# Performance work log

Hardware: AMD Instinct MI355X
Metric: run time of the kernel (lower is better)

## Reference

```python
import jax, jax.numpy as jnp
import numpy as np

NUM_CLASSES = 4
SMOOTH = 1e-05
W_DICE, W_CE, W_BOUND = 1.0, 1.0, 0.01
BIG = 1e8  # effectively-infinite squared distance


def _edt_sq_pass(f, axis):
    # Exact 1D squared-distance transform along `axis` via min-plus:
    # out[i] = min_j f[j] + (i-j)^2  (brute-force O(n^2), fully vectorized)
    n = f.shape[axis]
    i = jnp.arange(n, dtype=f.dtype)
    d2 = (i[:, None] - i[None, :]) ** 2  # [n, n]
    fm = jnp.moveaxis(f, axis, -1)
    out = jnp.min(fm[..., None, :] + d2, axis=-1)
    return jnp.moveaxis(out, -1, axis)


def _edt(zero_mask):
    # Euclidean distance to the nearest True voxel of zero_mask
    # (equivalent to scipy distance_transform_edt(~zero_mask)'s convention:
    #  distance to nearest zero of the input == nearest True of zero_mask).
    f = jnp.where(zero_mask, 0.0, BIG).astype(jnp.float32)
    for ax in range(f.ndim):
        f = _edt_sq_pass(f, ax)
    return jnp.sqrt(f)


def _signed_distance(mask):
    # mask: bool [D,H,W]; signed distance map: + outside, - inside.
    d_out = _edt(mask)            # distance(1 - mask)
    d_in = _edt(~mask)            # distance(mask)
    sdf = d_out - d_in
    total = jnp.sum(mask)
    size = mask.size
    sdf = jnp.where(total == 0, jnp.ones_like(sdf), sdf)
    sdf = jnp.where(total == size, -jnp.ones_like(sdf), sdf)
    return sdf


def setup_inputs() -> dict:
    key = jax.random.key(0)
    k1, k2 = jax.random.split(key)
    preds = jax.random.normal(k1, (4, NUM_CLASSES, 64, 64, 64), dtype=jnp.float32)
    targets = jax.random.randint(k2, (4, 64, 64, 64), 0, NUM_CLASSES, dtype=jnp.int32)
    return {"preds": preds, "targets": targets}


def reference(preds, targets):
    B = preds.shape[0]
    probs = jax.nn.softmax(preds, axis=1)  # [B,C,D,H,W]

    # --- Soft Dice ---
    onehot = jax.nn.one_hot(targets, NUM_CLASSES, dtype=preds.dtype)  # [B,D,H,W,C]
    onehot = jnp.moveaxis(onehot, -1, 1)  # [B,C,D,H,W]
    inter = jnp.sum(probs * onehot, axis=(2, 3, 4))
    union = jnp.sum(probs, axis=(2, 3, 4)) + jnp.sum(onehot, axis=(2, 3, 4))
    dice = (2.0 * inter + SMOOTH) / (union + SMOOTH)
    l_dice = 1.0 - jnp.mean(dice)

    # --- Cross entropy (mean over all voxels) ---
    logp = jax.nn.log_softmax(preds, axis=1)
    picked = jnp.take_along_axis(logp, targets[:, None].astype(jnp.int32), axis=1)
    l_ce = -jnp.mean(picked)

    # --- Boundary loss (classes 1..C-1) ---
    l_bound = jnp.float32(0.0)
    for c in range(1, NUM_CLASSES):
        mask_c = targets == c  # [B,D,H,W]
        sdf_c = jax.vmap(_signed_distance)(mask_c)  # [B,D,H,W]
        l_bound = l_bound + jnp.sum(jnp.mean(sdf_c * probs[:, c], axis=(1, 2, 3)))
    l_bound = l_bound / (B * (NUM_CLASSES - 1))

    return W_DICE * l_dice + W_CE * l_ce + W_BOUND * l_bound
```

## Files before the change

### kernel.cpp

```cpp
#include <hip/hip_runtime.h>
#include <hip/hip_bf16.h>
#include <math.h>

#define NVOX 262144
#define BIGF 1e8f
#define GRID_A 1024
#define GRID_B 768
#define GRID_K2 768

__device__ __forceinline__ unsigned short f2bf(float x) {
    __hip_bfloat16 h = __float2bfloat16(x);
    return *reinterpret_cast<unsigned short*>(&h);
}
__device__ __forceinline__ float bf2f(unsigned short u) {
    __hip_bfloat16 h = *reinterpret_cast<__hip_bfloat16*>(&u);
    return __bfloat162float(h);
}
__device__ __forceinline__ unsigned short dist2_u16(unsigned long long mask, int w) {
    if (mask == 0ull) return 0xFFFFu;
    unsigned long long mr = mask >> w;
    unsigned long long ml = mask << (63 - w);
    int dr = mr ? __builtin_ctzll(mr) : 127;
    int dl = ml ? __builtin_clzll(ml) : 127;
    int dd = dr < dl ? dr : dl;
    return (unsigned short)(dd * dd);
}

__global__ __launch_bounds__(256) void K1_fused(
    const float* __restrict__ preds, const int* __restrict__ targets,
    unsigned short* __restrict__ bufA, unsigned short* __restrict__ probsT,
    float* __restrict__ part_stats) {
    __shared__ float tO[64 * 65];
    __shared__ float tI[64 * 65];
    __shared__ float sred[4 * 13];
    int bid = blockIdx.x;
    int t = threadIdx.x, lane = t & 63, wid = t >> 6;

    if (bid < GRID_A) {
        int b = bid >> 8, seg = bid & 255;
        size_t vbase = (size_t)seg * 1024 + 4 * t;
        const float* p = preds + (size_t)(b * 4) * NVOX + vbase;
        float4 x0 = *(const float4*)(p);
        float4 x1 = *(const float4*)(p + NVOX);
        float4 x2 = *(const float4*)(p + 2 * NVOX);
        float4 x3 = *(const float4*)(p + 3 * NVOX);
        int4 tv4 = *(const int4*)(targets + (size_t)b * NVOX + vbase);

        float q[13];
        #pragma unroll
        for (int k = 0; k < 13; ++k) q[k] = 0.0f;
        unsigned short pb[3][4];

        #pragma unroll
        for (int j = 0; j < 4; ++j) {
            float a0 = (&x0.x)[j], a1 = (&x1.x)[j], a2 = (&x2.x)[j], a3 = (&x3.x)[j];
            int tv = (&tv4.x)[j];
            float m  = fmaxf(fmaxf(a0, a1), fmaxf(a2, a3));
            float e0 = expf(a0 - m), e1 = expf(a1 - m), e2 = expf(a2 - m), e3 = expf(a3 - m);
            float ssum = e0 + e1 + e2 + e3;
            float inv  = 1.0f / ssum;
            float p0 = e0 * inv, p1 = e1 * inv, p2 = e2 * inv, p3 = e3 * inv;
            float xt = (tv == 0) ? a0 : (tv == 1) ? a1 : (tv == 2) ? a2 : a3;
            q[12] += -(xt - m - logf(ssum));
            q[4] += p0; q[5] += p1; q[6] += p2; q[7] += p3;
            if (tv == 0)      { q[0] += p0; q[8]  += 1.0f; }
            else if (tv == 1) { q[1] += p1; q[9]  += 1.0f; }
            else if (tv == 2) { q[2] += p2; q[10] += 1.0f; }
            else              { q[3] += p3; q[11] += 1.0f; }
            pb[0][j] = f2bf(p1); pb[1][j] = f2bf(p2); pb[2][j] = f2bf(p3);
        }

        int v0 = (int)vbase;
        int d = v0 >> 12, h = (v0 >> 6) & 63, w0 = v0 & 63;
        size_t poff = (size_t)h * 4096 + d * 64 + w0;
        #pragma unroll
        for (int c = 0; c < 3; ++c) {
            ushort4 u = make_ushort4(pb[c][0], pb[c][1], pb[c][2], pb[c][3]);
            *(ushort4*)(probsT + (size_t)(b * 3 + c) * NVOX + poff) = u;
        }

        #pragma unroll
        for (int k = 0; k < 13; ++k) {
            float x = q[k];
            #pragma unroll
            for (int o = 32; o > 0; o >>= 1) x += __shfl_down(x, o);
            if (lane == 0) sred[wid * 13 + k] = x;
        }
        __syncthreads();
        if (t < 13) {
            float s = sred[t] + sred[13 + t] + sred[26 + t] + sred[39 + t];
            part_stats[t * 1024 + bid] = s;
        }
    } else {
        int blk = bid - GRID_A;
        int cm = blk % 3;
        int bd = blk / 3;
        int d = bd & 63, b = bd >> 6;
        int c = cm + 1;
        const int* tg = targets + (size_t)b * NVOX + (size_t)d * 4096;

        #pragma unroll
        for (int i = 0; i < 16; ++i) {
            int e = t + 256 * i;
            int h = wid + 4 * i;
            int tv = tg[e];
            unsigned long long mask = __ballot(tv == c);
            unsigned short o  = dist2_u16(mask, lane);
            unsigned short ii = dist2_u16(~mask, lane);
            tO[h * 65 + lane] = (o  == 0xFFFFu) ? BIGF : (float)o;
            tI[h * 65 + lane] = (ii == 0xFFFFu) ? BIGF : (float)ii;
        }
        __syncthreads();

        for (int r = 0; r < 16; ++r) {
            int w = wid * 16 + r;
            {
                float best = tO[lane * 65 + w];
                for (int dk = 1; dk < 64; ++dk) {
                    float d2 = (float)(dk * dk);
                    if (__all(d2 >= best)) break;
                    int hl = lane - dk; hl = hl < 0 ? 0 : hl;
                    int hr = lane + dk; hr = hr > 63 ? 63 : hr;
                    best = fminf(fminf(best, tO[hl * 65 + w] + d2), tO[hr * 65 + w] + d2);
                }
                tO[lane * 65 + w] = best;
            }
            {
                float best = tI[lane * 65 + w];
                for (int dk = 1; dk < 64; ++dk) {
                    float d2 = (float)(dk * dk);
                    if (__all(d2 >= best)) break;
                    int hl = lane - dk; hl = hl < 0 ? 0 : hl;
                    int hr = lane + dk; hr = hr > 63 ? 63 : hr;
                    best = fminf(fminf(best, tI[hl * 65 + w] + d2), tI[hr * 65 + w] + d2);
                }
                tI[lane * 65 + w] = best;
            }
        }
        __syncthreads();

        int combo = b * 3 + cm;
        size_t oO = (size_t)combo * NVOX + (size_t)d * 64;
        size_t oI = (size_t)(combo + 12) * NVOX + (size_t)d * 64;
        #pragma unroll
        for (int i = 0; i < 16; ++i) {
            int h = wid + 4 * i;
            float vo = tO[h * 65 + lane];
            float vi = tI[h * 65 + lane];
            bufA[oO + (size_t)h * 4096 + lane] = (vo >= 1e7f) ? 0xFFFFu : (unsigned short)vo;
            bufA[oI + (size_t)h * 4096 + lane] = (vi >= 1e7f) ? 0xFFFFu : (unsigned short)vi;
        }
    }
}

__global__ __launch_bounds__(512) void K2_edt3_sdf(
    const unsigned short* __restrict__ bufA, const unsigned short* __restrict__ probsT,
    float* __restrict__ part_bound) {
    __shared__ float pl[2][64 * 65];
    __shared__ float sredb[8];
    int blk = blockIdx.x;
    int combo = blk >> 6, h = blk & 63;
    int t = threadIdx.x, lane = t & 63, wid = t >> 6;

    for (int v = 0; v < 2; ++v) {
        const unsigned short* src = bufA + (size_t)(combo + 12 * v) * NVOX + (size_t)h * 4096;
        #pragma unroll
        for (int i = 0; i < 8; ++i) {
            int e = t + 512 * i;
            unsigned short u = src[e];
            pl[v][e + (e >> 6)] = (u == 0xFFFFu) ? BIGF : (float)u;
        }
    }
    __syncthreads();

    for (int v = 0; v < 2; ++v) {
        for (int r = 0; r < 8; ++r) {
            int w = wid * 8 + r;
            float* col = &pl[v][w];
            float best = col[lane * 65];
            for (int dk = 1; dk < 64; ++dk) {
                float d2 = (float)(dk * dk);
                if (__all(d2 >= best)) break;
                int dl = lane - dk; dl = dl < 0 ? 0 : dl;
                int dr = lane + dk; dr = dr > 63 ? 63 : dr;
                best = fminf(fminf(best, col[dl * 65] + d2), col[dr * 65] + d2);
            }
            col[lane * 65] = best;
        }
    }
    __syncthreads();

    const unsigned short* pp = probsT + (size_t)combo * NVOX + (size_t)h * 4096;
    float acc = 0.0f;
    #pragma unroll
    for (int i = 0; i < 8; ++i) {
        int e = t + 512 * i;
        int li = e + (e >> 6);
        float sdf = sqrtf(pl[0][li]) - sqrtf(pl[1][li]);
        acc += sdf * bf2f(pp[e]);
    }
    #pragma unroll
    for (int o = 32; o > 0; o >>= 1) acc += __shfl_down(acc, o);
    if (lane == 0) sredb[wid] = acc;
    __syncthreads();
    if (t == 0) {
        float s = 0.0f;
        for (int j = 0; j < 8; ++j) s += sredb[j];
        part_bound[blk] = s;
    }
}

__global__ __launch_bounds__(1024) void K3_final(
    const float* __restrict__ part_stats, const float* __restrict__ part_bound,
    float* __restrict__ out) {
    __shared__ float sred[13 * 16];
    __shared__ float bred[12];
    __shared__ double S[52];
    int t = threadIdx.x, lane = t & 63, wid = t >> 6;

    float v[13];
    #pragma unroll
    for (int k = 0; k < 13; ++k) v[k] = part_stats[k * 1024 + t];
    float bv = (wid < 12) ? part_bound[wid * 64 + lane] : 0.0f;

    #pragma unroll
    for (int k = 0; k < 13; ++k) {
        float x = v[k];
        #pragma unroll
        for (int o = 32; o > 0; o >>= 1) x += __shfl_down(x, o);
        if (lane == 0) sred[k * 16 + wid] = x;
    }
    #pragma unroll
    for (int o = 32; o > 0; o >>= 1) bv += __shfl_down(bv, o);
    if (lane == 0 && wid < 12) bred[wid] = bv;
    __syncthreads();

    if (t < 52) {
        int k = t >> 2, b = t & 3;
        S[k * 4 + b] = (double)sred[k * 16 + b * 4]     + (double)sred[k * 16 + b * 4 + 1]
                     + (double)sred[k * 16 + b * 4 + 2] + (double)sred[k * 16 + b * 4 + 3];
    }
    __syncthreads();
    if (t == 0) {
        const double NV = (double)NVOX;
        double dice_sum = 0.0;
        for (int b = 0; b < 4; ++b)
            for (int c = 0; c < 4; ++c) {
                double inter = S[c * 4 + b];
                double un    = S[(4 + c) * 4 + b] + S[(8 + c) * 4 + b];
                dice_sum += (2.0 * inter + 1e-5) / (un + 1e-5);
            }
        double l_dice = 1.0 - dice_sum / 16.0;
        double l_ce = (S[48] + S[49] + S[50] + S[51]) / (4.0 * NV);
        double lb = 0.0;
        for (int cb = 0; cb < 12; ++cb) {
            int b = cb / 3, c = cb % 3 + 1;
            double cnt = S[(8 + c) * 4 + b];
            double s;
            if (cnt == 0.0)      s =  S[(4 + c) * 4 + b];
            else if (cnt == NV)  s = -S[(4 + c) * 4 + b];
            else                 s =  (double)bred[cb];
            lb += s / NV;
        }
        lb /= 12.0;
        out[0] = (float)(l_dice + l_ce + 0.01 * lb);
    }
}

extern "C" void kernel_launch(void* const* d_in, const int* in_sizes, int n_in,
                              void* d_out, int out_size, void* d_ws, size_t ws_size,
                              hipStream_t stream) {
    const float* preds   = (const float*)d_in[0];
    const int*   targets = (const int*)d_in[1];
    float* out = (float*)d_out;

    unsigned short* bufA   = (unsigned short*)d_ws;
    unsigned short* probsT = bufA + (size_t)24 * NVOX;
    float* part_stats = (float*)(probsT + (size_t)12 * NVOX);
    float* part_bound = part_stats + 13 * 1024;

    K1_fused<<<GRID_A + GRID_B, 256, 0, stream>>>(preds, targets, bufA, probsT, part_stats);
    K2_edt3_sdf<<<GRID_K2, 512, 0, stream>>>(bufA, probsT, part_bound);
    K3_final<<<1, 1024, 0, stream>>>(part_stats, part_bound, out);
}
```

Baseline: 48.82 us.

## Split fused stats/EDT kernel into two launches with finer stats grid

Splits the combined softmax-stats and first-two-axis EDT kernel into two separate kernels. The stats kernel now processes 2 voxels per thread across 2048 blocks, and uses exp2f, log2f and the hardware reciprocal in place of expf, logf and division. The final reduction kernel is adapted to 2048 partial sums per statistic. The aim is more parallelism and cheaper transcendentals in the stats pass. In exchange the two workloads can no longer overlap inside one launch, and the extra kernel launch is serialized.

```diff
diff --git a/kernel.cpp b/kernel.cpp
--- a/kernel.cpp
+++ b/kernel.cpp
@@ -4,7 +4,7 @@
 
 #define NVOX 262144
 #define BIGF 1e8f
-#define GRID_A 1024
+#define GRID_A 2048
 #define GRID_B 768
 #define GRID_K2 768
 
@@ -26,130 +26,135 @@
     return (unsigned short)(dd * dd);
 }
 
-__global__ __launch_bounds__(256) void K1_fused(
+__global__ __launch_bounds__(256) void kA2_stats_probs(
     const float* __restrict__ preds, const int* __restrict__ targets,
-    unsigned short* __restrict__ bufA, unsigned short* __restrict__ probsT,
-    float* __restrict__ part_stats) {
+    unsigned short* __restrict__ probsT, float* __restrict__ part_stats) {
+    __shared__ float sred[4 * 13];
+    int bid = blockIdx.x;
+    int t = threadIdx.x, lane = t & 63, wid = t >> 6;
+    int g0 = bid * 512 + 2 * t;
+    int b = g0 >> 18;
+    int v0 = g0 & (NVOX - 1);
+    const float* p = preds + (size_t)(b * 4) * NVOX + v0;
+    float2 x0 = *(const float2*)(p);
+    float2 x1 = *(const float2*)(p + NVOX);
+    float2 x2 = *(const float2*)(p + 2 * NVOX);
+    float2 x3 = *(const float2*)(p + 3 * NVOX);
+    int2 tv2 = *(const int2*)(targets + (size_t)b * NVOX + v0);
+
+    const float L2E = 1.4426950408889634f;
+    const float LN2 = 0.6931471805599453f;
+    float q[13];
+    #pragma unroll
+    for (int k = 0; k < 13; ++k) q[k] = 0.0f;
+    unsigned short pb[3][2];
+
+    #pragma unroll
+    for (int j = 0; j < 2; ++j) {
+        float a0 = (&x0.x)[j], a1 = (&x1.x)[j], a2 = (&x2.x)[j], a3 = (&x3.x)[j];
+        int tv = (&tv2.x)[j];
+        float m  = fmaxf(fmaxf(a0, a1), fmaxf(a2, a3));
+        float e0 = exp2f((a0 - m) * L2E);
+        float e1 = exp2f((a1 - m) * L2E);
+        float e2 = exp2f((a2 - m) * L2E);
+        float e3 = exp2f((a3 - m) * L2E);
+        float ssum = e0 + e1 + e2 + e3;
+        float inv  = __builtin_amdgcn_rcpf(ssum);
+        float p0 = e0 * inv, p1 = e1 * inv, p2 = e2 * inv, p3 = e3 * inv;
+        float xt = (tv == 0) ? a0 : (tv == 1) ? a1 : (tv == 2) ? a2 : a3;
+        q[12] += (m - xt) + log2f(ssum) * LN2;
+        q[4] += p0; q[5] += p1; q[6] += p2; q[7] += p3;
+        if (tv == 0)      { q[0] += p0; q[8]  += 1.0f; }
+        else if (tv == 1) { q[1] += p1; q[9]  += 1.0f; }
+        else if (tv == 2) { q[2] += p2; q[10] += 1.0f; }
+        else              { q[3] += p3; q[11] += 1.0f; }
+        pb[0][j] = f2bf(p1); pb[1][j] = f2bf(p2); pb[2][j] = f2bf(p3);
+    }
+
+    int d = v0 >> 12, h = (v0 >> 6) & 63, w0 = v0 & 63;
+    size_t poff = (size_t)h * 4096 + d * 64 + w0;
+    #pragma unroll
+    for (int c = 0; c < 3; ++c) {
+        ushort2 u = make_ushort2(pb[c][0], pb[c][1]);
+        *(ushort2*)(probsT + (size_t)(b * 3 + c) * NVOX + poff) = u;
+    }
+
+    #pragma unroll
+    for (int k = 0; k < 13; ++k) {
+        float x = q[k];
+        #pragma unroll
+        for (int o = 32; o > 0; o >>= 1) x += __shfl_down(x, o);
+        if (lane == 0) sred[wid * 13 + k] = x;
+    }
+    __syncthreads();
+    if (t < 13) {
+        float s = sred[t] + sred[13 + t] + sred[26 + t] + sred[39 + t];
+        part_stats[t * 2048 + bid] = s;
+    }
+}
+
+__global__ __launch_bounds__(256) void kB_edt12(
+    const int* __restrict__ targets, unsigned short* __restrict__ bufA) {
     __shared__ float tO[64 * 65];
     __shared__ float tI[64 * 65];
-    __shared__ float sred[4 * 13];
-    int bid = blockIdx.x;
-    int t = threadIdx.x, lane = t & 63, wid = t >> 6;
-
-    if (bid < GRID_A) {
-        int b = bid >> 8, seg = bid & 255;
-        size_t vbase = (size_t)seg * 1024 + 4 * t;
-        const float* p = preds + (size_t)(b * 4) * NVOX + vbase;
-        float4 x0 = *(const float4*)(p);
-        float4 x1 = *(const float4*)(p + NVOX);
-        float4 x2 = *(const float4*)(p + 2 * NVOX);
-        float4 x3 = *(const float4*)(p + 3 * NVOX);
-        int4 tv4 = *(const int4*)(targets + (size_t)b * NVOX + vbase);
-
-        float q[13];
-        #pragma unroll
-        for (int k = 0; k < 13; ++k) q[k] = 0.0f;
-        unsigned short pb[3][4];
-
-        #pragma unroll
-        for (int j = 0; j < 4; ++j) {
-            float a0 = (&x0.x)[j], a1 = (&x1.x)[j], a2 = (&x2.x)[j], a3 = (&x3.x)[j];
-            int tv = (&tv4.x)[j];
-            float m  = fmaxf(fmaxf(a0, a1), fmaxf(a2, a3));
-            float e0 = expf(a0 - m), e1 = expf(a1 - m), e2 = expf(a2 - m), e3 = expf(a3 - m);
-            float ssum = e0 + e1 + e2 + e3;
-            float inv  = 1.0f / ssum;
-            float p0 = e0 * inv, p1 = e1 * inv, p2 = e2 * inv, p3 = e3 * inv;
-            float xt = (tv == 0) ? a0 : (tv == 1) ? a1 : (tv == 2) ? a2 : a3;
-            q[12] += -(xt - m - logf(ssum));
-            q[4] += p0; q[5] += p1; q[6] += p2; q[7] += p3;
-            if (tv == 0)      { q[0] += p0; q[8]  += 1.0f; }
-            else if (tv == 1) { q[1] += p1; q[9]  += 1.0f; }
-            else if (tv == 2) { q[2] += p2; q[10] += 1.0f; }
-            else              { q[3] += p3; q[11] += 1.0f; }
-            pb[0][j] = f2bf(p1); pb[1][j] = f2bf(p2); pb[2][j] = f2bf(p3);
-        }
-
-        int v0 = (int)vbase;
-        int d = v0 >> 12, h = (v0 >> 6) & 63, w0 = v0 & 63;
-        size_t poff = (size_t)h * 4096 + d * 64 + w0;
-        #pragma unroll
-        for (int c = 0; c < 3; ++c) {
-            ushort4 u = make_ushort4(pb[c][0], pb[c][1], pb[c][2], pb[c][3]);
-            *(ushort4*)(probsT + (size_t)(b * 3 + c) * NVOX + poff) = u;
-        }
-
-        #pragma unroll
-        for (int k = 0; k < 13; ++k) {
-            float x = q[k];
-            #pragma unroll
-            for (int o = 32; o > 0; o >>= 1) x += __shfl_down(x, o);
-            if (lane == 0) sred[wid * 13 + k] = x;
-        }
-        __syncthreads();
-        if (t < 13) {
-            float s = sred[t] + sred[13 + t] + sred[26 + t] + sred[39 + t];
-            part_stats[t * 1024 + bid] = s;
-        }
-    } else {
-        int blk = bid - GRID_A;
-        int cm = blk % 3;
-        int bd = blk / 3;
-        int d = bd & 63, b = bd >> 6;
-        int c = cm + 1;
-        const int* tg = targets + (size_t)b * NVOX + (size_t)d * 4096;
-
-        #pragma unroll
-        for (int i = 0; i < 16; ++i) {
-            int e = t + 256 * i;
-            int h = wid + 4 * i;
-            int tv = tg[e];
-            unsigned long long mask = __ballot(tv == c);
-            unsigned short o  = dist2_u16(mask, lane);
-            unsigned short ii = dist2_u16(~mask, lane);
-            tO[h * 65 + lane] = (o  == 0xFFFFu) ? BIGF : (float)o;
-            tI[h * 65 + lane] = (ii == 0xFFFFu) ? BIGF : (float)ii;
-        }
-        __syncthreads();
-
-        for (int r = 0; r < 16; ++r) {
-            int w = wid * 16 + r;
-            {
-                float best = tO[lane * 65 + w];
-                for (int dk = 1; dk < 64; ++dk) {
-                    float d2 = (float)(dk * dk);
-                    if (__all(d2 >= best)) break;
-                    int hl = lane - dk; hl = hl < 0 ? 0 : hl;
-                    int hr = lane + dk; hr = hr > 63 ? 63 : hr;
-                    best = fminf(fminf(best, tO[hl * 65 + w] + d2), tO[hr * 65 + w] + d2);
-                }
-                tO[lane * 65 + w] = best;
-            }
-            {
-                float best = tI[lane * 65 + w];
-                for (int dk = 1; dk < 64; ++dk) {
-                    float d2 = (float)(dk * dk);
-                    if (__all(d2 >= best)) break;
-                    int hl = lane - dk; hl = hl < 0 ? 0 : hl;
-                    int hr = lane + dk; hr = hr > 63 ? 63 : hr;
-                    best = fminf(fminf(best, tI[hl * 65 + w] + d2), tI[hr * 65 + w] + d2);
-                }
-                tI[lane * 65 + w] = best;
-            }
-        }
-        __syncthreads();
-
-        int combo = b * 3 + cm;
-        size_t oO = (size_t)combo * NVOX + (size_t)d * 64;
-        size_t oI = (size_t)(combo + 12) * NVOX + (size_t)d * 64;
-        #pragma unroll
-        for (int i = 0; i < 16; ++i) {
-            int h = wid + 4 * i;
-            float vo = tO[h * 65 + lane];
-            float vi = tI[h * 65 + lane];
-            bufA[oO + (size_t)h * 4096 + lane] = (vo >= 1e7f) ? 0xFFFFu : (unsigned short)vo;
-            bufA[oI + (size_t)h * 4096 + lane] = (vi >= 1e7f) ? 0xFFFFu : (unsigned short)vi;
-        }
+    int blk = blockIdx.x;
+    int cm = blk % 3;
+    int bd = blk / 3;
+    int d = bd & 63, b = bd >> 6;
+    int c = cm + 1;
+    int t = threadIdx.x, lane = t & 63, wid = t >> 6;
+    const int* tg = targets + (size_t)b * NVOX + (size_t)d * 4096;
+
+    #pragma unroll
+    for (int i = 0; i < 16; ++i) {
+        int e = t + 256 * i;
+        int h = wid + 4 * i;
+        int tv = tg[e];
+        unsigned long long mask = __ballot(tv == c);
+        unsigned short o  = dist2_u16(mask, lane);
+        unsigned short ii = dist2_u16(~mask, lane);
+        tO[h * 65 + lane] = (o  == 0xFFFFu) ? BIGF : (float)o;
+        tI[h * 65 + lane] = (ii == 0xFFFFu) ? BIGF : (float)ii;
+    }
+    __syncthreads();
+
+    for (int r = 0; r < 16; ++r) {
+        int w = wid * 16 + r;
+        {
+            float best = tO[lane * 65 + w];
+            for (int dk = 1; dk < 64; ++dk) {
+                float d2 = (float)(dk * dk);
+                if (__all(d2 >= best)) break;
+                int hl = lane - dk; hl = hl < 0 ? 0 : hl;
+                int hr = lane + dk; hr = hr > 63 ? 63 : hr;
+                best = fminf(fminf(best, tO[hl * 65 + w] + d2), tO[hr * 65 + w] + d2);
+            }
+            tO[lane * 65 + w] = best;
+        }
+        {
+            float best = tI[lane * 65 + w];
+            for (int dk = 1; dk < 64; ++dk) {
+                float d2 = (float)(dk * dk);
+                if (__all(d2 >= best)) break;
+                int hl = lane - dk; hl = hl < 0 ? 0 : hl;
+                int hr = lane + dk; hr = hr > 63 ? 63 : hr;
+                best = fminf(fminf(best, tI[hl * 65 + w] + d2), tI[hr * 65 + w] + d2);
+            }
+            tI[lane * 65 + w] = best;
+        }
+    }
+    __syncthreads();
+
+    int combo = b * 3 + cm;
+    size_t oO = (size_t)combo * NVOX + (size_t)d * 64;
+    size_t oI = (size_t)(combo + 12) * NVOX + (size_t)d * 64;
+    #pragma unroll
+    for (int i = 0; i < 16; ++i) {
+        int h = wid + 4 * i;
+        float vo = tO[h * 65 + lane];
+        float vi = tI[h * 65 + lane];
+        bufA[oO + (size_t)h * 4096 + lane] = (vo >= 1e7f) ? 0xFFFFu : (unsigned short)vo;
+        bufA[oI + (size_t)h * 4096 + lane] = (vi >= 1e7f) ? 0xFFFFu : (unsigned short)vi;
     }
 }
 
@@ -213,22 +218,26 @@
 __global__ __launch_bounds__(1024) void K3_final(
     const float* __restrict__ part_stats, const float* __restrict__ part_bound,
     float* __restrict__ out) {
-    __shared__ float sred[13 * 16];
+    __shared__ float sredA[13 * 16];
+    __shared__ float sredB[13 * 16];
     __shared__ float bred[12];
     __shared__ double S[52];
     int t = threadIdx.x, lane = t & 63, wid = t >> 6;
 
-    float v[13];
-    #pragma unroll
-    for (int k = 0; k < 13; ++k) v[k] = part_stats[k * 1024 + t];
+    float vA[13], vB[13];
+    #pragma unroll
+    for (int k = 0; k < 13; ++k) {
+        vA[k] = part_stats[k * 2048 + t];
+        vB[k] = part_stats[k * 2048 + 1024 + t];
+    }
     float bv = (wid < 12) ? part_bound[wid * 64 + lane] : 0.0f;
 
     #pragma unroll
     for (int k = 0; k < 13; ++k) {
-        float x = v[k];
+        float xa = vA[k], xb = vB[k];
         #pragma unroll
-        for (int o = 32; o > 0; o >>= 1) x += __shfl_down(x, o);
-        if (lane == 0) sred[k * 16 + wid] = x;
+        for (int o = 32; o > 0; o >>= 1) { xa += __shfl_down(xa, o); xb += __shfl_down(xb, o); }
+        if (lane == 0) { sredA[k * 16 + wid] = xa; sredB[k * 16 + wid] = xb; }
     }
     #pragma unroll
     for (int o = 32; o > 0; o >>= 1) bv += __shfl_down(bv, o);
@@ -236,9 +245,12 @@
     __syncthreads();
 
     if (t < 52) {
-        int k = t >> 2, b = t & 3;
-        S[k * 4 + b] = (double)sred[k * 16 + b * 4]     + (double)sred[k * 16 + b * 4 + 1]
-                     + (double)sred[k * 16 + b * 4 + 2] + (double)sred[k * 16 + b * 4 + 3];
+        int k = t >> 2, bsel = t & 3;
+        const float* src = (bsel < 2) ? sredA : sredB;
+        int base = k * 16 + (bsel & 1) * 8;
+        double s = 0.0;
+        for (int j = 0; j < 8; ++j) s += (double)src[base + j];
+        S[k * 4 + bsel] = s;
     }
     __syncthreads();
     if (t == 0) {
@@ -277,9 +289,10 @@
     unsigned short* bufA   = (unsigned short*)d_ws;
     unsigned short* probsT = bufA + (size_t)24 * NVOX;
     float* part_stats = (float*)(probsT + (size_t)12 * NVOX);
-    float* part_bound = part_stats + 13 * 1024;
-
-    K1_fused<<<GRID_A + GRID_B, 256, 0, stream>>>(preds, targets, bufA, probsT, part_stats);
+    float* part_bound = part_stats + 13 * 2048;
+
+    kA2_stats_probs<<<GRID_A, 256, 0, stream>>>(preds, targets, probsT, part_stats);
+    kB_edt12<<<GRID_B, 256, 0, stream>>>(targets, bufA);
     K2_edt3_sdf<<<GRID_K2, 512, 0, stream>>>(bufA, probsT, part_bound);
     K3_final<<<1, 1024, 0, stream>>>(part_stats, part_bound, out);
 }
```

After: 58.47 us. +19.8%, slower.

## Split fused K1 into probs, stats and EDT kernels with u16 shared tiles

Applied to the files above, without the earlier changes.

Splits the heterogeneous fused first kernel into three kernels: one writing the bf16 transposed probabilities, one computing the dice/CE statistics, and one doing the first two EDT passes. The EDT tiles move from float to unsigned short in shared memory, which halves LDS use. The 0xFFFF sentinel is now kept as 65535 rather than mapped to a large float. Softmax uses exp2f and the hardware reciprocal. The split re-reads preds twice and adds launch overhead. It also changes how the sentinel distance behaves in later passes, which risks wrong results when a class is absent in a row.

```diff
diff --git a/kernel.cpp b/kernel.cpp
--- a/kernel.cpp
+++ b/kernel.cpp
@@ -4,7 +4,6 @@
 
 #define NVOX 262144
 #define BIGF 1e8f
-#define GRID_A 1024
 #define GRID_B 768
 #define GRID_K2 768
 
@@ -26,130 +25,158 @@
     return (unsigned short)(dd * dd);
 }
 
-__global__ __launch_bounds__(256) void K1_fused(
+__global__ __launch_bounds__(256) void kA_probs(
+    const float* __restrict__ preds, unsigned short* __restrict__ probsT) {
+    int bid = blockIdx.x, t = threadIdx.x;
+    int g0 = bid * 1024 + 4 * t;
+    int b = g0 >> 18;
+    int v0 = g0 & (NVOX - 1);
+    const float* p = preds + (size_t)(b * 4) * NVOX + v0;
+    float4 x0 = *(const float4*)(p);
+    float4 x1 = *(const float4*)(p + NVOX);
+    float4 x2 = *(const float4*)(p + 2 * NVOX);
+    float4 x3 = *(const float4*)(p + 3 * NVOX);
+
+    const float L2E = 1.4426950408889634f;
+    unsigned short pb[3][4];
+    #pragma unroll
+    for (int j = 0; j < 4; ++j) {
+        float a0 = (&x0.x)[j], a1 = (&x1.x)[j], a2 = (&x2.x)[j], a3 = (&x3.x)[j];
+        float m  = fmaxf(fmaxf(a0, a1), fmaxf(a2, a3));
+        float e0 = exp2f((a0 - m) * L2E);
+        float e1 = exp2f((a1 - m) * L2E);
+        float e2 = exp2f((a2 - m) * L2E);
+        float e3 = exp2f((a3 - m) * L2E);
+        float inv = __builtin_amdgcn_rcpf(e0 + e1 + e2 + e3);
+        pb[0][j] = f2bf(e1 * inv);
+        pb[1][j] = f2bf(e2 * inv);
+        pb[2][j] = f2bf(e3 * inv);
+    }
+    int d = v0 >> 12, h = (v0 >> 6) & 63, w0 = v0 & 63;
+    size_t poff = (size_t)h * 4096 + d * 64 + w0;
+    #pragma unroll
+    for (int c = 0; c < 3; ++c) {
+        ushort4 u = make_ushort4(pb[c][0], pb[c][1], pb[c][2], pb[c][3]);
+        *(ushort4*)(probsT + (size_t)(b * 3 + c) * NVOX + poff) = u;
+    }
+}
+
+__global__ __launch_bounds__(256) void kA_stats(
     const float* __restrict__ preds, const int* __restrict__ targets,
-    unsigned short* __restrict__ bufA, unsigned short* __restrict__ probsT,
     float* __restrict__ part_stats) {
-    __shared__ float tO[64 * 65];
-    __shared__ float tI[64 * 65];
     __shared__ float sred[4 * 13];
-    int bid = blockIdx.x;
+    int bid = blockIdx.x, t = threadIdx.x, lane = t & 63, wid = t >> 6;
+    int g0 = bid * 1024 + 4 * t;
+    int b = g0 >> 18;
+    int v0 = g0 & (NVOX - 1);
+    const float* p = preds + (size_t)(b * 4) * NVOX + v0;
+    float4 x0 = *(const float4*)(p);
+    float4 x1 = *(const float4*)(p + NVOX);
+    float4 x2 = *(const float4*)(p + 2 * NVOX);
+    float4 x3 = *(const float4*)(p + 3 * NVOX);
+    int4 tv4 = *(const int4*)(targets + (size_t)b * NVOX + v0);
+
+    const float L2E = 1.4426950408889634f;
+    const float LN2 = 0.6931471805599453f;
+    float q[13];
+    #pragma unroll
+    for (int k = 0; k < 13; ++k) q[k] = 0.0f;
+
+    #pragma unroll
+    for (int j = 0; j < 4; ++j) {
+        float a0 = (&x0.x)[j], a1 = (&x1.x)[j], a2 = (&x2.x)[j], a3 = (&x3.x)[j];
+        int tv = (&tv4.x)[j];
+        float m  = fmaxf(fmaxf(a0, a1), fmaxf(a2, a3));
+        float e0 = exp2f((a0 - m) * L2E);
+        float e1 = exp2f((a1 - m) * L2E);
+        float e2 = exp2f((a2 - m) * L2E);
+        float e3 = exp2f((a3 - m) * L2E);
+        float ssum = e0 + e1 + e2 + e3;
+        float inv  = __builtin_amdgcn_rcpf(ssum);
+        float p0 = e0 * inv, p1 = e1 * inv, p2 = e2 * inv, p3 = e3 * inv;
+        float xt = (tv == 0) ? a0 : (tv == 1) ? a1 : (tv == 2) ? a2 : a3;
+        q[12] += (m - xt) + log2f(ssum) * LN2;
+        q[4] += p0; q[5] += p1; q[6] += p2; q[7] += p3;
+        if (tv == 0)      { q[0] += p0; q[8]  += 1.0f; }
+        else if (tv == 1) { q[1] += p1; q[9]  += 1.0f; }
+        else if (tv == 2) { q[2] += p2; q[10] += 1.0f; }
+        else              { q[3] += p3; q[11] += 1.0f; }
+    }
+
+    #pragma unroll
+    for (int k = 0; k < 13; ++k) {
+        float x = q[k];
+        #pragma unroll
+        for (int o = 32; o > 0; o >>= 1) x += __shfl_down(x, o);
+        if (lane == 0) sred[wid * 13 + k] = x;
+    }
+    __syncthreads();
+    if (t < 13) {
+        float s = sred[t] + sred[13 + t] + sred[26 + t] + sred[39 + t];
+        part_stats[t * 1024 + bid] = s;
+    }
+}
+
+__global__ __launch_bounds__(256) void kB_edt12(
+    const int* __restrict__ targets, unsigned short* __restrict__ bufA) {
+    __shared__ unsigned short tO[64 * 66];
+    __shared__ unsigned short tI[64 * 66];
+    int blk = blockIdx.x;
+    int cm = blk % 3;
+    int bd = blk / 3;
+    int d = bd & 63, b = bd >> 6;
+    int c = cm + 1;
     int t = threadIdx.x, lane = t & 63, wid = t >> 6;
-
-    if (bid < GRID_A) {
-        int b = bid >> 8, seg = bid & 255;
-        size_t vbase = (size_t)seg * 1024 + 4 * t;
-        const float* p = preds + (size_t)(b * 4) * NVOX + vbase;
-        float4 x0 = *(const float4*)(p);
-        float4 x1 = *(const float4*)(p + NVOX);
-        float4 x2 = *(const float4*)(p + 2 * NVOX);
-        float4 x3 = *(const float4*)(p + 3 * NVOX);
-        int4 tv4 = *(const int4*)(targets + (size_t)b * NVOX + vbase);
-
-        float q[13];
-        #pragma unroll
-        for (int k = 0; k < 13; ++k) q[k] = 0.0f;
-        unsigned short pb[3][4];
-
-        #pragma unroll
-        for (int j = 0; j < 4; ++j) {
-            float a0 = (&x0.x)[j], a1 = (&x1.x)[j], a2 = (&x2.x)[j], a3 = (&x3.x)[j];
-            int tv = (&tv4.x)[j];
-            float m  = fmaxf(fmaxf(a0, a1), fmaxf(a2, a3));
-            float e0 = expf(a0 - m), e1 = expf(a1 - m), e2 = expf(a2 - m), e3 = expf(a3 - m);
-            float ssum = e0 + e1 + e2 + e3;
-            float inv  = 1.0f / ssum;
-            float p0 = e0 * inv, p1 = e1 * inv, p2 = e2 * inv, p3 = e3 * inv;
-            float xt = (tv == 0) ? a0 : (tv == 1) ? a1 : (tv == 2) ? a2 : a3;
-            q[12] += -(xt - m - logf(ssum));
-            q[4] += p0; q[5] += p1; q[6] += p2; q[7] += p3;
-            if (tv == 0)      { q[0] += p0; q[8]  += 1.0f; }
-            else if (tv == 1) { q[1] += p1; q[9]  += 1.0f; }
-            else if (tv == 2) { q[2] += p2; q[10] += 1.0f; }
-            else              { q[3] += p3; q[11] += 1.0f; }
-            pb[0][j] = f2bf(p1); pb[1][j] = f2bf(p2); pb[2][j] = f2bf(p3);
-        }
-
-        int v0 = (int)vbase;
-        int d = v0 >> 12, h = (v0 >> 6) & 63, w0 = v0 & 63;
-        size_t poff = (size_t)h * 4096 + d * 64 + w0;
-        #pragma unroll
-        for (int c = 0; c < 3; ++c) {
-            ushort4 u = make_ushort4(pb[c][0], pb[c][1], pb[c][2], pb[c][3]);
-            *(ushort4*)(probsT + (size_t)(b * 3 + c) * NVOX + poff) = u;
-        }
-
-        #pragma unroll
-        for (int k = 0; k < 13; ++k) {
-            float x = q[k];
-            #pragma unroll
-            for (int o = 32; o > 0; o >>= 1) x += __shfl_down(x, o);
-            if (lane == 0) sred[wid * 13 + k] = x;
-        }
-        __syncthreads();
-        if (t < 13) {
-            float s = sred[t] + sred[13 + t] + sred[26 + t] + sred[39 + t];
-            part_stats[t * 1024 + bid] = s;
-        }
-    } else {
-        int blk = bid - GRID_A;
-        int cm = blk % 3;
-        int bd = blk / 3;
-        int d = bd & 63, b = bd >> 6;
-        int c = cm + 1;
-        const int* tg = targets + (size_t)b * NVOX + (size_t)d * 4096;
-
-        #pragma unroll
-        for (int i = 0; i < 16; ++i) {
-            int e = t + 256 * i;
-            int h = wid + 4 * i;
-            int tv = tg[e];
-            unsigned long long mask = __ballot(tv == c);
-            unsigned short o  = dist2_u16(mask, lane);
-            unsigned short ii = dist2_u16(~mask, lane);
-            tO[h * 65 + lane] = (o  == 0xFFFFu) ? BIGF : (float)o;
-            tI[h * 65 + lane] = (ii == 0xFFFFu) ? BIGF : (float)ii;
-        }
-        __syncthreads();
-
-        for (int r = 0; r < 16; ++r) {
-            int w = wid * 16 + r;
-            {
-                float best = tO[lane * 65 + w];
-                for (int dk = 1; dk < 64; ++dk) {
-                    float d2 = (float)(dk * dk);
-                    if (__all(d2 >= best)) break;
-                    int hl = lane - dk; hl = hl < 0 ? 0 : hl;
-                    int hr = lane + dk; hr = hr > 63 ? 63 : hr;
-                    best = fminf(fminf(best, tO[hl * 65 + w] + d2), tO[hr * 65 + w] + d2);
-                }
-                tO[lane * 65 + w] = best;
+    const int* tg = targets + (size_t)b * NVOX + (size_t)d * 4096;
+
+    #pragma unroll
+    for (int i = 0; i < 16; ++i) {
+        int e = t + 256 * i;
+        int h = wid + 4 * i;
+        int tv = tg[e];
+        unsigned long long mask = __ballot(tv == c);
+        tO[h * 66 + lane] = dist2_u16(mask, lane);
+        tI[h * 66 + lane] = dist2_u16(~mask, lane);
+    }
+    __syncthreads();
+
+    for (int r = 0; r < 16; ++r) {
+        int w = wid * 16 + r;
+        {
+            float best = (float)tO[lane * 66 + w];
+            for (int dk = 1; dk < 64; ++dk) {
+                float d2 = (float)(dk * dk);
+                if (__all(d2 >= best)) break;
+                int hl = lane - dk; hl = hl < 0 ? 0 : hl;
+                int hr = lane + dk; hr = hr > 63 ? 63 : hr;
+                best = fminf(fminf(best, (float)tO[hl * 66 + w] + d2),
+                             (float)tO[hr * 66 + w] + d2);
             }
-            {
-                float best = tI[lane * 65 + w];
-                for (int dk = 1; dk < 64; ++dk) {
-                    float d2 = (float)(dk * dk);
-                    if (__all(d2 >= best)) break;
-                    int hl = lane - dk; hl = hl < 0 ? 0 : hl;
-                    int hr = lane + dk; hr = hr > 63 ? 63 : hr;
-                    best = fminf(fminf(best, tI[hl * 65 + w] + d2), tI[hr * 65 + w] + d2);
-                }
-                tI[lane * 65 + w] = best;
+            tO[lane * 66 + w] = (unsigned short)best;
+        }
+        {
+            float best = (float)tI[lane * 66 + w];
+            for (int dk = 1; dk < 64; ++dk) {
+                float d2 = (float)(dk * dk);
+                if (__all(d2 >= best)) break;
+                int hl = lane - dk; hl = hl < 0 ? 0 : hl;
+                int hr = lane + dk; hr = hr > 63 ? 63 : hr;
+                best = fminf(fminf(best, (float)tI[hl * 66 + w] + d2),
+                             (float)tI[hr * 66 + w] + d2);
             }
-        }
-        __syncthreads();
-
-        int combo = b * 3 + cm;
-        size_t oO = (size_t)combo * NVOX + (size_t)d * 64;
-        size_t oI = (size_t)(combo + 12) * NVOX + (size_t)d * 64;
-        #pragma unroll
-        for (int i = 0; i < 16; ++i) {
-            int h = wid + 4 * i;
-            float vo = tO[h * 65 + lane];
-            float vi = tI[h * 65 + lane];
-            bufA[oO + (size_t)h * 4096 + lane] = (vo >= 1e7f) ? 0xFFFFu : (unsigned short)vo;
-            bufA[oI + (size_t)h * 4096 + lane] = (vi >= 1e7f) ? 0xFFFFu : (unsigned short)vi;
-        }
+            tI[lane * 66 + w] = (unsigned short)best;
+        }
+    }
+    __syncthreads();
+
+    int combo = b * 3 + cm;
+    size_t oO = (size_t)combo * NVOX + (size_t)d * 64;
+    size_t oI = (size_t)(combo + 12) * NVOX + (size_t)d * 64;
+    #pragma unroll
+    for (int i = 0; i < 16; ++i) {
+        int h = wid + 4 * i;
+        bufA[oO + (size_t)h * 4096 + lane] = tO[h * 66 + lane];
+        bufA[oI + (size_t)h * 4096 + lane] = tI[h * 66 + lane];
     }
 }
 
@@ -167,8 +194,7 @@
         #pragma unroll
         for (int i = 0; i < 8; ++i) {
             int e = t + 512 * i;
-            unsigned short u = src[e];
-            pl[v][e + (e >> 6)] = (u == 0xFFFFu) ? BIGF : (float)u;
+            pl[v][e + (e >> 6)] = (float)src[e];
         }
     }
     __syncthreads();
@@ -279,7 +305,9 @@
     float* part_stats = (float*)(probsT + (size_t)12 * NVOX);
     float* part_bound = part_stats + 13 * 1024;
 
-    K1_fused<<<GRID_A + GRID_B, 256, 0, stream>>>(preds, targets, bufA, probsT, part_stats);
+    kA_probs<<<1024, 256, 0, stream>>>(preds, probsT);
+    kA_stats<<<1024, 256, 0, stream>>>(preds, targets, part_stats);
+    kB_edt12<<<GRID_B, 256, 0, stream>>>(targets, bufA);
     K2_edt3_sdf<<<GRID_K2, 512, 0, stream>>>(bufA, probsT, part_bound);
     K3_final<<<1, 1024, 0, stream>>>(part_stats, part_bound, out);
 }
```

Result: slower. 56.46 us (+15.6%).
